# Kernel tuning notes

Hardware: AMD Instinct MI355X
Metric: run time of the kernel (lower is better)

Reference implementation:

```python
import jax, jax.numpy as jnp
import numpy as np

B, T, NV, DEG, E = 64, 256, 20000, 8, 128
NSEG, NBUCKET = NV * DEG, 288
F_DIST, F_DIR, F_TT, HID = 50, 50, 50, 100
FEED = 2 * E + F_DIST + F_DIR  # 356


def setup_inputs() -> dict:
    key = jax.random.key(0)
    ks = jax.random.split(key, 32)
    s = 1.0 / np.sqrt(E)
    return {
        "xs_padded": jax.random.randint(ks[0], (B, T), 0, NV),
        "lengths": jax.random.randint(ks[1], (B,), 8, T + 1),
        "xs_actions": jax.random.randint(ks[2], (B, T - 1), 0, DEG),
        "destinations": jax.random.randint(ks[3], (B,), 0, NV),
        "adj_list": jax.random.randint(ks[4], (NV, DEG), 0, NV),
        "seg_ids": jax.random.randint(ks[5], (NV, DEG), 0, NSEG),
        "start_time": 42,
        "locations": jax.random.normal(ks[6], (NV, 2)),
        "time_dist_seg": jax.random.uniform(ks[7], (NSEG, NBUCKET)) * 10.0,
        "emb": jax.random.normal(ks[8], (NV + 2, E)) * 0.01,
        "Wq": jax.random.normal(ks[9], (E, E)) * s,
        "Wk": jax.random.normal(ks[10], (E, E)) * s,
        "Wv": jax.random.normal(ks[11], (E, E)) * s,
        "Wo": jax.random.normal(ks[12], (E, E)) * s,
        "dist_W": jax.random.normal(ks[13], (1, F_DIST)),
        "dist_b": jnp.zeros((F_DIST,)),
        "dir_W": jax.random.normal(ks[14], (2, F_DIR)) * 0.7,
        "dir_b": jnp.zeros((F_DIR,)),
        "tt_W": jax.random.normal(ks[15], (1, F_TT)),
        "tt_b": jnp.zeros((F_TT,)),
        "ob_W1": jax.random.normal(ks[16], (F_TT, F_TT // 2)) * (1.0 / np.sqrt(F_TT)),
        "ob_b1": jnp.zeros((F_TT // 2,)),
        "ob_W2": jax.random.normal(ks[17], (F_TT // 2, 1)) * (1.0 / np.sqrt(F_TT // 2)),
        "ob_b2": jnp.zeros((1,)),
        "om_W1": jax.random.normal(ks[18], (FEED, HID)) * (1.0 / np.sqrt(FEED)),
        "om_b1": jnp.zeros((HID,)),
        "om_W2": jax.random.normal(ks[19], (HID, HID // 2)) * (1.0 / np.sqrt(HID)),
        "om_b2": jnp.zeros((HID // 2,)),
        "om_W3": jax.random.normal(ks[20], (HID // 2, 1)) * (1.0 / np.sqrt(HID // 2)),
        "om_b3": jnp.zeros((1,)),
    }


def reference(xs_padded, lengths, xs_actions, destinations, adj_list, seg_ids,
              start_time, locations, time_dist_seg, emb, Wq, Wk, Wv, Wo,
              dist_W, dist_b, dir_W, dir_b, tt_W, tt_b,
              ob_W1, ob_b1, ob_W2, ob_b2,
              om_W1, om_b1, om_W2, om_b2, om_W3, om_b3):
    # --- embeddings + causal/padding-masked self-attention (flash_att) ---
    x_e = emb[xs_padded]                                       # [B,T,E]
    q, k, v = x_e @ Wq, x_e @ Wk, x_e @ Wv
    scores = jnp.einsum('bqe,bke->bqk', q, k) / jnp.sqrt(jnp.float32(E))
    causal = jnp.triu(jnp.ones((T, T), bool), 1)
    pad = jnp.arange(T)[None, :] >= lengths[:, None]           # key padding [B,T]
    scores = jnp.where(causal[None] | pad[:, None, :], -1e9, scores)
    hidden = jnp.einsum('bqk,bke->bqe', jax.nn.softmax(scores, axis=-1), v) @ Wo

    # --- irregular neighbor gather: route_neighbors only filled for t < len-1 ---
    valid_t = jnp.arange(T)[None, :] < (lengths - 1)[:, None]  # [B,T]
    rn = jnp.where(valid_t[:, :, None], adj_list[xs_padded], 0)  # [B,T,DEG]

    # --- distance to destination feature ---
    dest_c = locations[destinations][:, None, None, :]         # [B,1,1,2]
    nbr_c = locations[rn]                                      # [B,T,DEG,2]
    dist = jnp.abs(nbr_c - dest_c).sum(-1, keepdims=True) * 100.0
    dist_f = dist @ dist_W + dist_b

    # --- direction (unit vector) feature ---
    vec = nbr_c - locations[xs_padded][:, :, None, :]
    unit = vec / (jnp.linalg.norm(vec, axis=-1, keepdims=True) + 1e-8)
    dir_f = unit @ dir_W + dir_b

    # --- travel-time lookup + masked whitening ---
    nmask = rn != 0
    tt = time_dist_seg[seg_ids[xs_padded], start_time]         # [B,T,DEG]
    mf = nmask.astype(tt.dtype)
    cnt = mf.sum()
    mean = (tt * mf).sum() / cnt
    var = (((tt - mean) ** 2) * mf).sum() / (cnt - 1.0)        # unbiased, like torch.std
    tt = (tt - mean) / (jnp.sqrt(var) + 1e-6)
    tt_f = (tt[..., None] @ tt_W + tt_b) * mf[..., None]

    # --- fuse and score neighbors ---
    hid_e = jnp.broadcast_to(hidden[:, :, None, :], (B, T, DEG, E))
    dest_e = jnp.broadcast_to(emb[destinations][:, None, None, :], (B, T, DEG, E))
    feed = jnp.concatenate([hid_e, dist_f, dir_f, dest_e], axis=-1)  # [B,T,DEG,356]

    ob = (jax.nn.relu(tt_f @ ob_W1 + ob_b1) @ ob_W2 + ob_b2).squeeze(-1)
    h1 = jax.nn.relu(feed @ om_W1 + om_b1)
    h2 = jax.nn.relu(h1 @ om_W2 + om_b2)
    logits = (h2 @ om_W3 + om_b3).squeeze(-1) + ob             # [B,T,DEG]

    # --- per-route mean cross-entropy over valid transitions, summed over batch ---
    logp = jax.nn.log_softmax(logits[:, :T - 1], axis=-1)
    nll = -jnp.take_along_axis(logp, xs_actions[..., None], axis=-1).squeeze(-1)
    vmask = (jnp.arange(T - 1)[None, :] < (lengths - 1)[:, None]).astype(nll.dtype)
    per = (nll * vmask).sum(1) / (lengths - 1).astype(nll.dtype)
    return per.sum()
```

## Files before the change

### kernel.cpp

```cpp
#include <hip/hip_runtime.h>
#include <math.h>

#define BB 64
#define TT 256
#define DEG 8
#define EE 128
#define NBUCKET 288
#define HID 100
#define H2 50

constexpr size_t OFF_STATS   = 0;
constexpr size_t OFF_CDIST   = 4;
constexpr size_t OFF_CDIRX   = 104;
constexpr size_t OFF_CDIRY   = 204;
constexpr size_t OFF_BASE    = 304;
constexpr size_t OFF_V25     = 404;
constexpr size_t OFF_C25     = 429;
constexpr size_t OFF_OBZ     = 454;
constexpr size_t OFF_DESTPRE = 456;
constexpr size_t OFF_WF      = 6856;
constexpr size_t OFF_TT      = 32456;
constexpr size_t OFF_Q       = 163528;
constexpr size_t OFF_K       = OFF_Q + 16384 * 128;
constexpr size_t OFF_VP      = OFF_K + 16384 * 128;

__global__ void __launch_bounds__(256) k_setup(
    const int* destinations, const float* emb, const float* Wo,
    const float* dist_W, const float* dist_b, const float* dir_W, const float* dir_b,
    const float* tt_W, const float* tt_b, const float* ob_W1, const float* ob_b1,
    const float* ob_W2, const float* ob_b2, const float* om_W1, const float* om_b1,
    float* ws, float* out) {
    __shared__ float sh[EE];
    int blk = blockIdx.x;
    int j = threadIdx.x;
    if (blk == 0) {
        if (j < 4) ws[OFF_STATS + j] = 0.f;
        if (j == 0) out[0] = 0.f;
        if (j < HID) {
            float cd = 0.f, cx = 0.f, cy = 0.f, bs = om_b1[j];
            for (int f = 0; f < 50; f++) {
                float w1d = om_W1[(128 + f) * HID + j];
                float w1r = om_W1[(178 + f) * HID + j];
                cd += dist_W[f] * w1d;
                bs += dist_b[f] * w1d + dir_b[f] * w1r;
                cx += dir_W[f] * w1r;
                cy += dir_W[50 + f] * w1r;
            }
            ws[OFF_CDIST + j] = cd; ws[OFF_CDIRX + j] = cx;
            ws[OFF_CDIRY + j] = cy; ws[OFF_BASE + j] = bs;
        }
        if (j >= 128 && j < 153) {
            int jj = j - 128;
            float v = 0.f, c = ob_b1[jj];
            for (int i = 0; i < 50; i++) {
                v += tt_W[i] * ob_W1[i * 25 + jj];
                c += tt_b[i] * ob_W1[i * 25 + jj];
            }
            ws[OFF_V25 + jj] = v; ws[OFF_C25 + jj] = c;
        }
        if (j == 200) {
            float z = ob_b2[0];
            for (int i = 0; i < 25; i++) z += fmaxf(ob_b1[i], 0.f) * ob_W2[i];
            ws[OFF_OBZ] = z;
        }
    } else if (blk <= 64) {
        int b = blk - 1;
        if (j < EE) sh[j] = emb[(size_t)destinations[b] * EE + j];
        __syncthreads();
        if (j < HID) {
            float acc = 0.f;
            for (int i = 0; i < EE; i++) acc += sh[i] * om_W1[(228 + i) * HID + j];
            ws[OFF_DESTPRE + b * HID + j] = acc;
        }
    } else {
        int i = blk - 65;
        if (j < EE) sh[j] = Wo[i * EE + j];
        __syncthreads();
        if (j < HID) {
            float acc = 0.f;
            for (int jj = 0; jj < EE; jj++) acc += sh[jj] * om_W1[jj * HID + j];
            ws[OFF_WF + i * HID + j] = acc;
        }
    }
}

__global__ void __launch_bounds__(256) k_mid(
    const int* xs, const int* lengths, const int* adj, const int* seg,
    const int* stime, const float* tds, const float* emb,
    const float* Wq, const float* Wk, const float* Wv, float* ws) {
    __shared__ float smem[2 * 128 * 36 + 32];
    int blk = blockIdx.x;
    int tid = threadIdx.x;
    if (blk < 512) {
        float (*XT)[36]  = (float(*)[36])smem;
        float (*T1T)[36] = (float(*)[36])(smem + 128 * 36);
        int* vids = (int*)(smem + 2 * 128 * 36);
        int r0 = blk * 32;
        if (tid < 32) vids[tid] = xs[r0 + tid];
        __syncthreads();
        for (int c = 0; c < 16; c++) {
            int idx = c * 256 + tid;
            int r = idx >> 7, i = idx & 127;
            XT[i][r] = emb[(size_t)vids[r] * EE + i];
        }
        __syncthreads();
        int cg = tid & 31, rg = tid >> 5;
        const float* Wmats[2] = {Wq, Wk};
        float* Omats[2] = {ws + OFF_Q, ws + OFF_K};
        for (int mtx = 0; mtx < 2; mtx++) {
            const float* W = Wmats[mtx];
            float acc[4][4];
            #pragma unroll
            for (int a = 0; a < 4; a++)
                #pragma unroll
                for (int bb = 0; bb < 4; bb++) acc[a][bb] = 0.f;
            #pragma unroll 4
            for (int i = 0; i < EE; i++) {
                float4 av = *(const float4*)&XT[i][rg << 2];
                float4 wv = *(const float4*)&W[i * EE + (cg << 2)];
                acc[0][0] += av.x * wv.x; acc[0][1] += av.x * wv.y; acc[0][2] += av.x * wv.z; acc[0][3] += av.x * wv.w;
                acc[1][0] += av.y * wv.x; acc[1][1] += av.y * wv.y; acc[1][2] += av.y * wv.z; acc[1][3] += av.y * wv.w;
                acc[2][0] += av.z * wv.x; acc[2][1] += av.z * wv.y; acc[2][2] += av.z * wv.z; acc[2][3] += av.z * wv.w;
                acc[3][0] += av.w * wv.x; acc[3][1] += av.w * wv.y; acc[3][2] += av.w * wv.z; acc[3][3] += av.w * wv.w;
            }
            float* O = Omats[mtx];
            #pragma unroll
            for (int jj = 0; jj < 4; jj++)
                *(float4*)&O[(size_t)(r0 + (rg << 2) + jj) * EE + (cg << 2)] =
                    make_float4(acc[jj][0], acc[jj][1], acc[jj][2], acc[jj][3]);
        }
        {
            float acc[4][4];
            #pragma unroll
            for (int a = 0; a < 4; a++)
                #pragma unroll
                for (int bb = 0; bb < 4; bb++) acc[a][bb] = 0.f;
            #pragma unroll 4
            for (int i = 0; i < EE; i++) {
                float4 av = *(const float4*)&XT[i][rg << 2];
                float4 wv = *(const float4*)&Wv[i * EE + (cg << 2)];
                acc[0][0] += av.x * wv.x; acc[0][1] += av.x * wv.y; acc[0][2] += av.x * wv.z; acc[0][3] += av.x * wv.w;
                acc[1][0] += av.y * wv.x; acc[1][1] += av.y * wv.y; acc[1][2] += av.y * wv.z; acc[1][3] += av.y * wv.w;
                acc[2][0] += av.z * wv.x; acc[2][1] += av.z * wv.y; acc[2][2] += av.z * wv.z; acc[2][3] += av.z * wv.w;
                acc[3][0] += av.w * wv.x; acc[3][1] += av.w * wv.y; acc[3][2] += av.w * wv.z; acc[3][3] += av.w * wv.w;
            }
            #pragma unroll
            for (int jj = 0; jj < 4; jj++)
                #pragma unroll
                for (int ii = 0; ii < 4; ii++)
                    T1T[(cg << 2) + ii][(rg << 2) + jj] = acc[jj][ii];
        }
        __syncthreads();
        if (cg < 25) {
            const float* WF = ws + OFF_WF;
            float acc[4][4];
            #pragma unroll
            for (int a = 0; a < 4; a++)
                #pragma unroll
                for (int bb = 0; bb < 4; bb++) acc[a][bb] = 0.f;
            #pragma unroll 4
            for (int i = 0; i < EE; i++) {
                float4 av = *(const float4*)&T1T[i][rg << 2];
                float4 wv = *(const float4*)&WF[i * HID + (cg << 2)];
                acc[0][0] += av.x * wv.x; acc[0][1] += av.x * wv.y; acc[0][2] += av.x * wv.z; acc[0][3] += av.x * wv.w;
                acc[1][0] += av.y * wv.x; acc[1][1] += av.y * wv.y; acc[1][2] += av.y * wv.z; acc[1][3] += av.y * wv.w;
                acc[2][0] += av.z * wv.x; acc[2][1] += av.z * wv.y; acc[2][2] += av.z * wv.z; acc[2][3] += av.z * wv.w;
                acc[3][0] += av.w * wv.x; acc[3][1] += av.w * wv.y; acc[3][2] += av.w * wv.z; acc[3][3] += av.w * wv.w;
            }
            float* VP = ws + OFF_VP;
            #pragma unroll
            for (int jj = 0; jj < 4; jj++)
                *(float4*)&VP[(size_t)(r0 + (rg << 2) + jj) * HID + (cg << 2)] =
                    make_float4(acc[jj][0], acc[jj][1], acc[jj][2], acc[jj][3]);
        }
    } else {
        float* rs = smem; float* rq = smem + 256; float* rc = smem + 512;
        int st = *stime;
        float lsum = 0.f, lsq = 0.f, lcnt = 0.f;
        int total = BB * TT * DEG;
        for (int idx = (blk - 512) * 256 + tid; idx < total; idx += 256 * 256) {
            int d = idx & 7;
            int bt = idx >> 3;
            int t = bt & 255;
            int b = bt >> 8;
            int len = lengths[b];
            if (t >= len - 1) continue;
            int v = xs[bt];
            int sg = seg[v * DEG + d];
            float tt = tds[(size_t)sg * NBUCKET + st];
            ws[OFF_TT + idx] = tt;
            int a = adj[v * DEG + d];
            if (a != 0) { lsum += tt; lsq += tt * tt; lcnt += 1.f; }
        }
        rs[tid] = lsum; rq[tid] = lsq; rc[tid] = lcnt;
        __syncthreads();
        for (int s = 128; s > 0; s >>= 1) {
            if (tid < s) { rs[tid] += rs[tid + s]; rq[tid] += rq[tid + s]; rc[tid] += rc[tid + s]; }
            __syncthreads();
        }
        if (tid == 0) {
            atomicAdd(&ws[OFF_STATS + 0], rs[0]);
            atomicAdd(&ws[OFF_STATS + 1], rq[0]);
            atomicAdd(&ws[OFF_STATS + 2], rc[0]);
        }
    }
}

__global__ void __launch_bounds__(256) k_attnfinal(
    const int* lengths, const int* xs, const int* xs_actions,
    const int* destinations, const int* adj, const float* locations,
    const float* om_W2, const float* om_b2, const float* om_W3, const float* om_b3,
    const float* ob_W2, const float* ob_b2,
    float* ws, float* out) {
    int b = blockIdx.x >> 4;
    int tile = blockIdx.x & 15;
    int t0 = tile << 4;
    int len = lengths[b];
    if (t0 >= len - 1) return;
    int nqv = len - 1 - t0; if (nqv > 16) nqv = 16;
    int nk = t0 + 16;
    int nm = nk >> 4;
    __shared__ float smem[17696];
    float (*S)[260]  = (float(*)[260])smem;
    float (*Qs)[132] = (float(*)[132])(smem + 4160);
    float* KV = smem + 6272;
    int tid = threadIdx.x;
    if (tid < 16) smem[17680 + tid] = 0.f;
    const float* Q  = ws + OFF_Q;
    const float* K  = ws + OFF_K;
    const float* VP = ws + OFF_VP;
    {
        const float* Qg = Q + ((size_t)(b * TT + t0)) * EE;
        for (int idx = tid; idx < 512; idx += 256) {
            int r = idx >> 5, c4 = (idx & 31) << 2;
            *(float4*)&Qs[r][c4] = *(const float4*)&Qg[r * EE + c4];
        }
    }
    int q = tid >> 4, li = tid & 15;
    int tq = t0 + q;
    float sreg[16];
    #pragma unroll
    for (int m = 0; m < 16; m++) sreg[m] = -1e30f;
    float (*Ks)[136] = (float(*)[136])KV;
    int ktend = ((nk + 31) >> 5) << 5;
    for (int kt = 0; kt < ktend; kt += 32) {
        __syncthreads();
        const float* Kg = K + ((size_t)(b * TT + kt)) * EE;
        for (int idx = tid; idx < 1024; idx += 256) {
            int r = idx >> 5, c4 = (idx & 31) << 2;
            *(float4*)&Ks[r][c4] = *(const float4*)&Kg[r * EE + c4];
        }
        __syncthreads();
        int k0 = kt + li, k1 = kt + li + 16;
        float s0 = 0.f, s1 = 0.f;
        const float4* q4  = (const float4*)Qs[q];
        const float4* k4a = (const float4*)Ks[li];
        const float4* k4b = (const float4*)Ks[li + 16];
        #pragma unroll 8
        for (int i = 0; i < 32; i++) {
            float4 a = q4[i];
            float4 x = k4a[i];
            float4 y = k4b[i];
            s0 += a.x * x.x + a.y * x.y + a.z * x.z + a.w * x.w;
            s1 += a.x * y.x + a.y * y.y + a.z * y.z + a.w * y.w;
        }
        int m0 = kt >> 4;
        if (k0 < nk && k0 <= tq) sreg[m0]     = s0 * 0.08838834764831845f;
        if (k1 < nk && k1 <= tq) sreg[m0 + 1] = s1 * 0.08838834764831845f;
    }
    float mx = -1e30f;
    for (int m = 0; m < nm; m++) mx = fmaxf(mx, sreg[m]);
    #pragma unroll
    for (int o = 1; o < 16; o <<= 1) mx = fmaxf(mx, __shfl_xor(mx, o, 16));
    float lsum = 0.f;
    for (int m = 0; m < nm; m++) { float p = __expf(sreg[m] - mx); sreg[m] = p; lsum += p; }
    #pragma unroll
    for (int o = 1; o < 16; o <<= 1) lsum += __shfl_xor(lsum, o, 16);
    float inv = 1.f / lsum;
    for (int m = 0; m < nm; m++) S[q][li + (m << 4)] = sreg[m];
    float acc[7];
    #pragma unroll
    for (int j = 0; j < 7; j++) acc[j] = 0.f;
    float (*Vs)[104] = (float(*)[104])KV;
    for (int vt = 0; vt < nk; vt += 32) {
        __syncthreads();
        const float* Vg = VP + ((size_t)(b * TT + vt)) * HID;
        for (int idx = tid; idx < 800; idx += 256) {
            int r = idx / 25, c4 = (idx - r * 25) << 2;
            *(float4*)&Vs[r][c4] = *(const float4*)&Vg[r * HID + c4];
        }
        __syncthreads();
        int kmax = nk - vt; if (kmax > 32) kmax = 32;
        for (int k = 0; k < kmax; k++) {
            float p = S[q][vt + k];
            #pragma unroll
            for (int j = 0; j < 7; j++) {
                int c = li + (j << 4);
                if (c < HID) acc[j] += p * Vs[k][c];
            }
        }
    }
    __syncthreads();
    {
        const float* BASEv = ws + OFF_BASE;
        const float* DP = ws + OFF_DESTPRE + b * HID;
        #pragma unroll
        for (int j = 0; j < 7; j++) {
            int c = li + (j << 4);
            if (c < HID) S[q][c] = acc[j] * inv + BASEv[c] + DP[c];
        }
    }
    float (*W2s)[64] = (float(*)[64])(smem + 4160);
    for (int idx = tid; idx < 6400; idx += 256) {
        int mm = idx >> 6, n = idx & 63;
        W2s[mm][n] = (n < H2) ? om_W2[mm * H2 + n] : 0.f;
    }
    float smean, sdinv;
    {
        float sum = ws[OFF_STATS], sq = ws[OFF_STATS + 1], cnt = ws[OFF_STATS + 2];
        smean = sum / cnt;
        float var = (sq - cnt * smean * smean) / (cnt - 1.f);
        sdinv = 1.f / (sqrtf(var) + 1e-6f);
    }
    float (*h1T)[68] = (float(*)[68])(smem + 10560);
    float* distR = smem + 17360;
    float* uxR   = smem + 17424;
    float* uyR   = smem + 17488;
    float* obR   = smem + 17552;
    float* lgS   = smem + 17616;
    float* nllS  = smem + 17680;
    int cg = tid & 7, rg = tid >> 3;
    float b2v[8], w3v[8];
    #pragma unroll
    for (int k = 0; k < 8; k++) {
        int n = (cg << 3) + k;
        b2v[k] = (n < H2) ? om_b2[n] : 0.f;
        w3v[k] = (n < H2) ? om_W3[n] : 0.f;
    }
    float ob2s = ob_b2[0];
    float obz = ws[OFF_OBZ];
    __syncthreads();
    for (int qh = 0; qh < 2; qh++) {
        if (tid < 64) {
            int ql = tid >> 3, d = tid & 7;
            int qa = (qh << 3) + ql;
            int t = t0 + qa;
            int bt = b * TT + t;
            int v = xs[bt];
            int a = adj[v * DEG + d];
            float nbx = locations[2 * a], nby = locations[2 * a + 1];
            int dst = destinations[b];
            float dxl = locations[2 * dst], dyl = locations[2 * dst + 1];
            float cxl = locations[2 * v], cyl = locations[2 * v + 1];
            distR[tid] = (fabsf(nbx - dxl) + fabsf(nby - dyl)) * 100.f;
            float vx = nbx - cxl, vy = nby - cyl;
            float nrm = sqrtf(vx * vx + vy * vy) + 1e-8f;
            uxR[tid] = vx / nrm; uyR[tid] = vy / nrm;
            float ttn = (ws[OFF_TT + (size_t)bt * 8 + d] - smean) * sdinv;
            float obp = 0.f;
            for (int j = 0; j < 25; j++)
                obp += fmaxf(ttn * ws[OFF_V25 + j] + ws[OFF_C25 + j], 0.f) * ob_W2[j];
            obR[tid] = (a != 0) ? (obp + ob2s) : obz;
        }
        __syncthreads();
        {
            int r = tid & 63, mq = tid >> 6;
            int qa = (qh << 3) + (r >> 3);
            float dv = distR[r], ux = uxR[r], uy = uyR[r];
            const float* CD = ws + OFF_CDIST;
            const float* CX = ws + OFF_CDIRX;
            const float* CY = ws + OFF_CDIRY;
            const float* Hq = S[qa];
            int m0 = mq * 25;
            #pragma unroll 5
            for (int mi = 0; mi < 25; mi++) {
                int m = m0 + mi;
                float pre = Hq[m] + dv * CD[m] + ux * CX[m] + uy * CY[m];
                h1T[m][r] = fmaxf(pre, 0.f);
            }
        }
        __syncthreads();
        {
            float facc[2][8];
            #pragma unroll
            for (int jr = 0; jr < 2; jr++)
                #pragma unroll
                for (int k = 0; k < 8; k++) facc[jr][k] = 0.f;
            int r0 = rg << 1, n0 = cg << 3;
            #pragma unroll 4
            for (int m = 0; m < HID; m++) {
                float2 hv = *(const float2*)&h1T[m][r0];
                float4 w0 = *(const float4*)&W2s[m][n0];
                float4 w1 = *(const float4*)&W2s[m][n0 + 4];
                facc[0][0] += hv.x * w0.x; facc[0][1] += hv.x * w0.y;
                facc[0][2] += hv.x * w0.z; facc[0][3] += hv.x * w0.w;
                facc[0][4] += hv.x * w1.x; facc[0][5] += hv.x * w1.y;
                facc[0][6] += hv.x * w1.z; facc[0][7] += hv.x * w1.w;
                facc[1][0] += hv.y * w0.x; facc[1][1] += hv.y * w0.y;
                facc[1][2] += hv.y * w0.z; facc[1][3] += hv.y * w0.w;
                facc[1][4] += hv.y * w1.x; facc[1][5] += hv.y * w1.y;
                facc[1][6] += hv.y * w1.z; facc[1][7] += hv.y * w1.w;
            }
            #pragma unroll
            for (int jr = 0; jr < 2; jr++) {
                float part = 0.f;
                #pragma unroll
                for (int k = 0; k < 8; k++)
                    part += fmaxf(facc[jr][k] + b2v[k], 0.f) * w3v[k];
                part += __shfl_xor(part, 1, 64);
                part += __shfl_xor(part, 2, 64);
                part += __shfl_xor(part, 4, 64);
                if (cg == 0) {
                    int row = r0 + jr;
                    lgS[row] = part + om_b3[0] + obR[row];
                }
            }
        }
        __syncthreads();
        if (tid < 8) {
            int qa = (qh << 3) + tid;
            if (qa < nqv) {
                int t = t0 + qa;
                float lg[8];
                float mxl = -1e30f;
                #pragma unroll
                for (int d = 0; d < 8; d++) {
                    lg[d] = lgS[(tid << 3) + d];
                    mxl = fmaxf(mxl, lg[d]);
                }
                int act = xs_actions[b * (TT - 1) + t];
                float se = 0.f, sel = 0.f;
                #pragma unroll
                for (int d = 0; d < 8; d++) {
                    se += __expf(lg[d] - mxl);
                    if (d == act) sel = lg[d];
                }
                float nll = mxl + __logf(se) - sel;
                nllS[qa] = nll / (float)(len - 1);
            }
        }
        __syncthreads();
    }
    if (tid == 0) {
        float s = 0.f;
        #pragma unroll
        for (int i = 0; i < 16; i++) s += nllS[i];
        atomicAdd(out, s);
    }
}

extern "C" void kernel_launch(void* const* d_in, const int* in_sizes, int n_in,
                              void* d_out, int out_size, void* d_ws, size_t ws_size,
                              hipStream_t stream) {
    const int* xs_padded    = (const int*)d_in[0];
    const int* lengths      = (const int*)d_in[1];
    const int* xs_actions   = (const int*)d_in[2];
    const int* destinations = (const int*)d_in[3];
    const int* adj_list     = (const int*)d_in[4];
    const int* seg_ids      = (const int*)d_in[5];
    const int* start_time   = (const int*)d_in[6];
    const float* locations  = (const float*)d_in[7];
    const float* tds        = (const float*)d_in[8];
    const float* emb        = (const float*)d_in[9];
    const float* Wq         = (const float*)d_in[10];
    const float* Wk         = (const float*)d_in[11];
    const float* Wv         = (const float*)d_in[12];
    const float* Wo         = (const float*)d_in[13];
    const float* dist_W     = (const float*)d_in[14];
    const float* dist_b     = (const float*)d_in[15];
    const float* dir_W      = (const float*)d_in[16];
    const float* dir_b      = (const float*)d_in[17];
    const float* tt_W       = (const float*)d_in[18];
    const float* tt_b       = (const float*)d_in[19];
    const float* ob_W1      = (const float*)d_in[20];
    const float* ob_b1      = (const float*)d_in[21];
    const float* ob_W2      = (const float*)d_in[22];
    const float* ob_b2      = (const float*)d_in[23];
    const float* om_W1      = (const float*)d_in[24];
    const float* om_b1      = (const float*)d_in[25];
    const float* om_W2      = (const float*)d_in[26];
    const float* om_b2      = (const float*)d_in[27];
    const float* om_W3      = (const float*)d_in[28];
    const float* om_b3      = (const float*)d_in[29];
    float* ws  = (float*)d_ws;
    float* out = (float*)d_out;

    k_setup<<<193, 256, 0, stream>>>(destinations, emb, Wo, dist_W, dist_b,
                                     dir_W, dir_b, tt_W, tt_b, ob_W1, ob_b1,
                                     ob_W2, ob_b2, om_W1, om_b1, ws, out);
    k_mid<<<768, 256, 0, stream>>>(xs_padded, lengths, adj_list, seg_ids,
                                   start_time, tds, emb, Wq, Wk, Wv, ws);
    k_attnfinal<<<BB * 16, 256, 0, stream>>>(
        lengths, xs_padded, xs_actions, destinations, adj_list, locations,
        om_W2, om_b2, om_W3, om_b3, ob_W2, ob_b2, ws, out);
}
```

Measured before the change: 471.5 us.

## Halve attention query tile, reorder blocks longest-first, restructure QK and PV work split

```diff
diff --git a/kernel.cpp b/kernel.cpp
--- a/kernel.cpp
+++ b/kernel.cpp
@@ -212,107 +212,142 @@
     const float* om_W2, const float* om_b2, const float* om_W3, const float* om_b3,
     const float* ob_W2, const float* ob_b2,
     float* ws, float* out) {
-    int b = blockIdx.x >> 4;
-    int tile = blockIdx.x & 15;
-    int t0 = tile << 4;
+    int blk = blockIdx.x;
+    int tile = 31 - (blk >> 6);
+    int b = blk & 63;
+    int t0 = tile << 3;
     int len = lengths[b];
     if (t0 >= len - 1) return;
-    int nqv = len - 1 - t0; if (nqv > 16) nqv = 16;
-    int nk = t0 + 16;
-    int nm = nk >> 4;
-    __shared__ float smem[17696];
-    float (*S)[260]  = (float(*)[260])smem;
-    float (*Qs)[132] = (float(*)[132])(smem + 4160);
-    float* KV = smem + 6272;
+    int nqv = len - 1 - t0; if (nqv > 8) nqv = 8;
+    int nk = t0 + 8;
+    __shared__ float smem[13160];
+    float (*H1P)[104] = (float(*)[104])smem;
+    float (*Qs)[132]  = (float(*)[132])(smem + 832);
+    float (*S)[260]   = (float(*)[260])(smem + 1888);
+    float (*Vs)[104]  = (float(*)[104])(smem + 3968);
+    float (*pacc)[8]  = (float(*)[8])(smem + 10624);
+    float (*W2s)[56]  = (float(*)[56])(smem + 832);
+    float (*h1T)[64]  = (float(*)[64])(smem + 6432);
+    float* distR = smem + 12832;
+    float* uxR   = smem + 12896;
+    float* uyR   = smem + 12960;
+    float* obR   = smem + 13024;
+    float* lgS   = smem + 13088;
+    float* nllS  = smem + 13152;
     int tid = threadIdx.x;
-    if (tid < 16) smem[17680 + tid] = 0.f;
-    const float* Q  = ws + OFF_Q;
-    const float* K  = ws + OFF_K;
-    const float* VP = ws + OFF_VP;
+    if (tid < 8) nllS[tid] = 0.f;
     {
-        const float* Qg = Q + ((size_t)(b * TT + t0)) * EE;
-        for (int idx = tid; idx < 512; idx += 256) {
-            int r = idx >> 5, c4 = (idx & 31) << 2;
-            *(float4*)&Qs[r][c4] = *(const float4*)&Qg[r * EE + c4];
-        }
-    }
-    int q = tid >> 4, li = tid & 15;
-    int tq = t0 + q;
-    float sreg[16];
-    #pragma unroll
-    for (int m = 0; m < 16; m++) sreg[m] = -1e30f;
-    float (*Ks)[136] = (float(*)[136])KV;
-    int ktend = ((nk + 31) >> 5) << 5;
-    for (int kt = 0; kt < ktend; kt += 32) {
-        __syncthreads();
-        const float* Kg = K + ((size_t)(b * TT + kt)) * EE;
-        for (int idx = tid; idx < 1024; idx += 256) {
-            int r = idx >> 5, c4 = (idx & 31) << 2;
-            *(float4*)&Ks[r][c4] = *(const float4*)&Kg[r * EE + c4];
-        }
-        __syncthreads();
-        int k0 = kt + li, k1 = kt + li + 16;
-        float s0 = 0.f, s1 = 0.f;
-        const float4* q4  = (const float4*)Qs[q];
-        const float4* k4a = (const float4*)Ks[li];
-        const float4* k4b = (const float4*)Ks[li + 16];
-        #pragma unroll 8
-        for (int i = 0; i < 32; i++) {
-            float4 a = q4[i];
-            float4 x = k4a[i];
-            float4 y = k4b[i];
-            s0 += a.x * x.x + a.y * x.y + a.z * x.z + a.w * x.w;
-            s1 += a.x * y.x + a.y * y.y + a.z * y.z + a.w * y.w;
-        }
-        int m0 = kt >> 4;
-        if (k0 < nk && k0 <= tq) sreg[m0]     = s0 * 0.08838834764831845f;
-        if (k1 < nk && k1 <= tq) sreg[m0 + 1] = s1 * 0.08838834764831845f;
-    }
-    float mx = -1e30f;
-    for (int m = 0; m < nm; m++) mx = fmaxf(mx, sreg[m]);
-    #pragma unroll
-    for (int o = 1; o < 16; o <<= 1) mx = fmaxf(mx, __shfl_xor(mx, o, 16));
-    float lsum = 0.f;
-    for (int m = 0; m < nm; m++) { float p = __expf(sreg[m] - mx); sreg[m] = p; lsum += p; }
-    #pragma unroll
-    for (int o = 1; o < 16; o <<= 1) lsum += __shfl_xor(lsum, o, 16);
-    float inv = 1.f / lsum;
-    for (int m = 0; m < nm; m++) S[q][li + (m << 4)] = sreg[m];
-    float acc[7];
-    #pragma unroll
-    for (int j = 0; j < 7; j++) acc[j] = 0.f;
-    float (*Vs)[104] = (float(*)[104])KV;
-    for (int vt = 0; vt < nk; vt += 32) {
-        __syncthreads();
-        const float* Vg = VP + ((size_t)(b * TT + vt)) * HID;
-        for (int idx = tid; idx < 800; idx += 256) {
-            int r = idx / 25, c4 = (idx - r * 25) << 2;
-            *(float4*)&Vs[r][c4] = *(const float4*)&Vg[r * HID + c4];
-        }
-        __syncthreads();
-        int kmax = nk - vt; if (kmax > 32) kmax = 32;
-        for (int k = 0; k < kmax; k++) {
-            float p = S[q][vt + k];
-            #pragma unroll
-            for (int j = 0; j < 7; j++) {
-                int c = li + (j << 4);
-                if (c < HID) acc[j] += p * Vs[k][c];
-            }
-        }
+        const float* Qg = ws + OFF_Q + (size_t)(b * TT + t0) * EE;
+        int r = tid >> 5, c4 = (tid & 31) << 2;
+        *(float4*)&Qs[r][c4] = *(const float4*)&Qg[r * EE + c4];
     }
     __syncthreads();
     {
-        const float* BASEv = ws + OFF_BASE;
-        const float* DP = ws + OFF_DESTPRE + b * HID;
-        #pragma unroll
-        for (int j = 0; j < 7; j++) {
-            int c = li + (j << 4);
-            if (c < HID) S[q][c] = acc[j] * inv + BASEv[c] + DP[c];
-        }
-    }
-    float (*W2s)[64] = (float(*)[64])(smem + 4160);
-    for (int idx = tid; idx < 6400; idx += 256) {
-        int mm = idx >> 6, n = idx & 63;
+        const float* Kg = ws + OFF_K + (size_t)(b * TT) * EE;
+        int w = tid >> 6;
+        int key = (tid >> 2) & 15, chunk = tid & 3;
+        int coff = chunk << 5;
+        for (int k0 = w << 4; k0 < nk; k0 += 64) {
+            int kk = k0 + key;
+            if (kk < nk) {
+                float4 kf[8];
+                const float4* Kr = (const float4*)&Kg[(size_t)kk * EE + coff];
+                #pragma unroll
+                for (int j = 0; j < 8; j++) kf[j] = Kr[j];
+                #pragma unroll
+                for (int q = 0; q < 8; q++) {
+                    const float4* qr = (const float4*)&Qs[q][coff];
+                    float s = 0.f;
+                    #pragma unroll
+                    for (int j = 0; j < 8; j++) {
+                        float4 a = qr[j], x = kf[j];
+                        s += a.x * x.x + a.y * x.y + a.z * x.z + a.w * x.w;
+                    }
+                    s += __shfl_xor(s, 1, 64);
+                    s += __shfl_xor(s, 2, 64);
+                    if (chunk == 0) S[q][kk] = s * 0.08838834764831845f;
+                }
+            }
+        }
+    }
+    __syncthreads();
+    if (tid < 128) {
+        int q = tid >> 4, li = tid & 15;
+        int tq = t0 + q;
+        float sreg[16];
+        float mx = -1e30f;
+        #pragma unroll
+        for (int m = 0; m < 16; m++) {
+            int k = li + (m << 4);
+            float sv = (k < nk && k <= tq) ? S[q][k] : -1e30f;
+            sreg[m] = sv;
+            mx = fmaxf(mx, sv);
+        }
+        #pragma unroll
+        for (int o = 1; o < 16; o <<= 1) mx = fmaxf(mx, __shfl_xor(mx, o, 16));
+        float ls = 0.f;
+        #pragma unroll
+        for (int m = 0; m < 16; m++) {
+            float p = __expf(sreg[m] - mx);
+            sreg[m] = p; ls += p;
+        }
+        #pragma unroll
+        for (int o = 1; o < 16; o <<= 1) ls += __shfl_xor(ls, o, 16);
+        float inv = 1.f / ls;
+        #pragma unroll
+        for (int m = 0; m < 16; m++) S[q][li + (m << 4)] = sreg[m] * inv;
+    }
+    __syncthreads();
+    {
+        int kc = tid >> 7;
+        int q = (tid >> 4) & 7, cg = tid & 15;
+        float acc[8];
+        #pragma unroll
+        for (int j = 0; j < 8; j++) acc[j] = 0.f;
+        const float* VPg = ws + OFF_VP + (size_t)(b * TT) * HID;
+        for (int vt0 = 0; vt0 < nk; vt0 += 64) {
+            __syncthreads();
+            int nrow = nk - vt0; if (nrow > 64) nrow = 64;
+            for (int idx = tid; idx < nrow * 25; idx += 256) {
+                int r = idx / 25, c4 = (idx - r * 25) << 2;
+                *(float4*)&Vs[r][c4] = *(const float4*)&VPg[(size_t)(vt0 + r) * HID + c4];
+            }
+            __syncthreads();
+            int base = vt0 + (kc << 5);
+            int kmax = nk - base; if (kmax > 32) kmax = 32;
+            if (cg < 13) {
+                for (int k = 0; k < kmax; k++) {
+                    float p = S[q][base + k];
+                    const float4* vr = (const float4*)&Vs[(kc << 5) + k][cg << 3];
+                    float4 v0 = vr[0], v1 = vr[1];
+                    acc[0] += p * v0.x; acc[1] += p * v0.y;
+                    acc[2] += p * v0.z; acc[3] += p * v0.w;
+                    acc[4] += p * v1.x; acc[5] += p * v1.y;
+                    acc[6] += p * v1.z; acc[7] += p * v1.w;
+                }
+            }
+        }
+        if (kc == 1 && cg < 13) {
+            float* pp = pacc[(q << 4) + cg];
+            #pragma unroll
+            for (int j = 0; j < 8; j++) pp[j] = acc[j];
+        }
+        __syncthreads();
+        if (kc == 0 && cg < 13) {
+            const float* pp = pacc[(q << 4) + cg];
+            const float* BASEv = ws + OFF_BASE;
+            const float* DP = ws + OFF_DESTPRE + b * HID;
+            int c0 = cg << 3;
+            #pragma unroll
+            for (int j = 0; j < 8; j++) {
+                int c = c0 + j;
+                if (c < HID) H1P[q][c] = acc[j] + pp[j] + BASEv[c] + DP[c];
+            }
+        }
+    }
+    __syncthreads();
+    for (int idx = tid; idx < 5600; idx += 256) {
+        int mm = idx / 56, n = idx - mm * 56;
         W2s[mm][n] = (n < H2) ? om_W2[mm * H2 + n] : 0.f;
     }
     float smean, sdinv;
@@ -322,129 +357,121 @@
         float var = (sq - cnt * smean * smean) / (cnt - 1.f);
         sdinv = 1.f / (sqrtf(var) + 1e-6f);
     }
-    float (*h1T)[68] = (float(*)[68])(smem + 10560);
-    float* distR = smem + 17360;
-    float* uxR   = smem + 17424;
-    float* uyR   = smem + 17488;
-    float* obR   = smem + 17552;
-    float* lgS   = smem + 17616;
-    float* nllS  = smem + 17680;
-    int cg = tid & 7, rg = tid >> 3;
-    float b2v[8], w3v[8];
-    #pragma unroll
-    for (int k = 0; k < 8; k++) {
-        int n = (cg << 3) + k;
-        b2v[k] = (n < H2) ? om_b2[n] : 0.f;
-        w3v[k] = (n < H2) ? om_W3[n] : 0.f;
-    }
-    float ob2s = ob_b2[0];
-    float obz = ws[OFF_OBZ];
-    __syncthreads();
-    for (int qh = 0; qh < 2; qh++) {
-        if (tid < 64) {
-            int ql = tid >> 3, d = tid & 7;
-            int qa = (qh << 3) + ql;
-            int t = t0 + qa;
-            int bt = b * TT + t;
-            int v = xs[bt];
-            int a = adj[v * DEG + d];
-            float nbx = locations[2 * a], nby = locations[2 * a + 1];
-            int dst = destinations[b];
-            float dxl = locations[2 * dst], dyl = locations[2 * dst + 1];
-            float cxl = locations[2 * v], cyl = locations[2 * v + 1];
-            distR[tid] = (fabsf(nbx - dxl) + fabsf(nby - dyl)) * 100.f;
-            float vx = nbx - cxl, vy = nby - cyl;
-            float nrm = sqrtf(vx * vx + vy * vy) + 1e-8f;
-            uxR[tid] = vx / nrm; uyR[tid] = vy / nrm;
-            float ttn = (ws[OFF_TT + (size_t)bt * 8 + d] - smean) * sdinv;
-            float obp = 0.f;
-            for (int j = 0; j < 25; j++)
-                obp += fmaxf(ttn * ws[OFF_V25 + j] + ws[OFF_C25 + j], 0.f) * ob_W2[j];
-            obR[tid] = (a != 0) ? (obp + ob2s) : obz;
-        }
-        __syncthreads();
-        {
-            int r = tid & 63, mq = tid >> 6;
-            int qa = (qh << 3) + (r >> 3);
-            float dv = distR[r], ux = uxR[r], uy = uyR[r];
-            const float* CD = ws + OFF_CDIST;
-            const float* CX = ws + OFF_CDIRX;
-            const float* CY = ws + OFF_CDIRY;
-            const float* Hq = S[qa];
-            int m0 = mq * 25;
-            #pragma unroll 5
-            for (int mi = 0; mi < 25; mi++) {
-                int m = m0 + mi;
-                float pre = Hq[m] + dv * CD[m] + ux * CX[m] + uy * CY[m];
-                h1T[m][r] = fmaxf(pre, 0.f);
-            }
-        }
-        __syncthreads();
-        {
-            float facc[2][8];
-            #pragma unroll
-            for (int jr = 0; jr < 2; jr++)
+    if (tid < 64) {
+        int ql = tid >> 3, d = tid & 7;
+        int t = t0 + ql;
+        int bt = b * TT + t;
+        int v = xs[bt];
+        int a = adj[v * DEG + d];
+        float nbx = locations[2 * a], nby = locations[2 * a + 1];
+        int dst = destinations[b];
+        float dxl = locations[2 * dst], dyl = locations[2 * dst + 1];
+        float cxl = locations[2 * v], cyl = locations[2 * v + 1];
+        distR[tid] = (fabsf(nbx - dxl) + fabsf(nby - dyl)) * 100.f;
+        float vx = nbx - cxl, vy = nby - cyl;
+        float nrm = sqrtf(vx * vx + vy * vy) + 1e-8f;
+        uxR[tid] = vx / nrm; uyR[tid] = vy / nrm;
+        float ttn = (ws[OFF_TT + (size_t)bt * 8 + d] - smean) * sdinv;
+        float obp = 0.f;
+        for (int j = 0; j < 25; j++)
+            obp += fmaxf(ttn * ws[OFF_V25 + j] + ws[OFF_C25 + j], 0.f) * ob_W2[j];
+        obR[tid] = (a != 0) ? (obp + ob_b2[0]) : ws[OFF_OBZ];
+    }
+    __syncthreads();
+    {
+        int r = tid & 63, mq = tid >> 6;
+        int qa = r >> 3;
+        float dv = distR[r], ux = uxR[r], uy = uyR[r];
+        const float* CD = ws + OFF_CDIST;
+        const float* CX = ws + OFF_CDIRX;
+        const float* CY = ws + OFF_CDIRY;
+        const float* Hq = H1P[qa];
+        int m0 = mq * 25;
+        #pragma unroll 5
+        for (int mi = 0; mi < 25; mi++) {
+            int m = m0 + mi;
+            float pre = Hq[m] + dv * CD[m] + ux * CX[m] + uy * CY[m];
+            h1T[m][r] = fmaxf(pre, 0.f);
+        }
+    }
+    __syncthreads();
+    if (tid < 128) {
+        int rg = tid >> 3, cg = tid & 7;
+        int r0 = rg << 2, n0 = cg << 3;
+        float parts[4] = {0.f, 0.f, 0.f, 0.f};
+        if (cg < 7) {
+            float facc[4][8];
+            #pragma unroll
+            for (int jr = 0; jr < 4; jr++)
                 #pragma unroll
                 for (int k = 0; k < 8; k++) facc[jr][k] = 0.f;
-            int r0 = rg << 1, n0 = cg << 3;
             #pragma unroll 4
             for (int m = 0; m < HID; m++) {
-                float2 hv = *(const float2*)&h1T[m][r0];
+                float4 hv = *(const float4*)&h1T[m][r0];
                 float4 w0 = *(const float4*)&W2s[m][n0];
                 float4 w1 = *(const float4*)&W2s[m][n0 + 4];
-                facc[0][0] += hv.x * w0.x; facc[0][1] += hv.x * w0.y;
-                facc[0][2] += hv.x * w0.z; facc[0][3] += hv.x * w0.w;
-                facc[0][4] += hv.x * w1.x; facc[0][5] += hv.x * w1.y;
-                facc[0][6] += hv.x * w1.z; facc[0][7] += hv.x * w1.w;
-                facc[1][0] += hv.y * w0.x; facc[1][1] += hv.y * w0.y;
-                facc[1][2] += hv.y * w0.z; facc[1][3] += hv.y * w0.w;
-                facc[1][4] += hv.y * w1.x; facc[1][5] += hv.y * w1.y;
-                facc[1][6] += hv.y * w1.z; facc[1][7] += hv.y * w1.w;
-            }
-            #pragma unroll
-            for (int jr = 0; jr < 2; jr++) {
+                facc[0][0] += hv.x * w0.x; facc[0][1] += hv.x * w0.y; facc[0][2] += hv.x * w0.z; facc[0][3] += hv.x * w0.w;
+                facc[0][4] += hv.x * w1.x; facc[0][5] += hv.x * w1.y; facc[0][6] += hv.x * w1.z; facc[0][7] += hv.x * w1.w;
+                facc[1][0] += hv.y * w0.x; facc[1][1] += hv.y * w0.y; facc[1][2] += hv.y * w0.z; facc[1][3] += hv.y * w0.w;
+                facc[1][4] += hv.y * w1.x; facc[1][5] += hv.y * w1.y; facc[1][6] += hv.y * w1.z; facc[1][7] += hv.y * w1.w;
+                facc[2][0] += hv.z * w0.x; facc[2][1] += hv.z * w0.y; facc[2][2] += hv.z * w0.z; facc[2][3] += hv.z * w0.w;
+                facc[2][4] += hv.z * w1.x; facc[2][5] += hv.z * w1.y; facc[2][6] += hv.z * w1.z; facc[2][7] += hv.z * w1.w;
+                facc[3][0] += hv.w * w0.x; facc[3][1] += hv.w * w0.y; facc[3][2] += hv.w * w0.z; facc[3][3] += hv.w * w0.w;
+                facc[3][4] += hv.w * w1.x; facc[3][5] += hv.w * w1.y; facc[3][6] += hv.w * w1.z; facc[3][7] += hv.w * w1.w;
+            }
+            float b2v[8], w3v[8];
+            #pragma unroll
+            for (int k = 0; k < 8; k++) {
+                int n = n0 + k;
+                b2v[k] = (n < H2) ? om_b2[n] : 0.f;
+                w3v[k] = (n < H2) ? om_W3[n] : 0.f;
+            }
+            #pragma unroll
+            for (int jr = 0; jr < 4; jr++) {
                 float part = 0.f;
                 #pragma unroll
                 for (int k = 0; k < 8; k++)
                     part += fmaxf(facc[jr][k] + b2v[k], 0.f) * w3v[k];
-                part += __shfl_xor(part, 1, 64);
-                part += __shfl_xor(part, 2, 64);
-                part += __shfl_xor(part, 4, 64);
-                if (cg == 0) {
-                    int row = r0 + jr;
-                    lgS[row] = part + om_b3[0] + obR[row];
-                }
-            }
-        }
-        __syncthreads();
-        if (tid < 8) {
-            int qa = (qh << 3) + tid;
-            if (qa < nqv) {
-                int t = t0 + qa;
-                float lg[8];
-                float mxl = -1e30f;
-                #pragma unroll
-                for (int d = 0; d < 8; d++) {
-                    lg[d] = lgS[(tid << 3) + d];
-                    mxl = fmaxf(mxl, lg[d]);
-                }
-                int act = xs_actions[b * (TT - 1) + t];
-                float se = 0.f, sel = 0.f;
-                #pragma unroll
-                for (int d = 0; d < 8; d++) {
-                    se += __expf(lg[d] - mxl);
-                    if (d == act) sel = lg[d];
-                }
-                float nll = mxl + __logf(se) - sel;
-                nllS[qa] = nll / (float)(len - 1);
-            }
-        }
-        __syncthreads();
-    }
+                parts[jr] = part;
+            }
+        }
+        float ob3 = om_b3[0];
+        #pragma unroll
+        for (int jr = 0; jr < 4; jr++) {
+            float part = parts[jr];
+            part += __shfl_xor(part, 1, 64);
+            part += __shfl_xor(part, 2, 64);
+            part += __shfl_xor(part, 4, 64);
+            if (cg == 0) lgS[r0 + jr] = part + ob3 + obR[r0 + jr];
+        }
+    }
+    __syncthreads();
+    if (tid < 8) {
+        int qa = tid;
+        if (qa < nqv) {
+            float lg[8];
+            float mxl = -1e30f;
+            #pragma unroll
+            for (int d = 0; d < 8; d++) {
+                lg[d] = lgS[(qa << 3) + d];
+                mxl = fmaxf(mxl, lg[d]);
+            }
+            int act = xs_actions[b * (TT - 1) + t0 + qa];
+            float se = 0.f, sel = 0.f;
+            #pragma unroll
+            for (int d = 0; d < 8; d++) {
+                se += __expf(lg[d] - mxl);
+                if (d == act) sel = lg[d];
+            }
+            float nll = mxl + __logf(se) - sel;
+            nllS[qa] = nll / (float)(len - 1);
+        }
+    }
+    __syncthreads();
     if (tid == 0) {
         float s = 0.f;
         #pragma unroll
-        for (int i = 0; i < 16; i++) s += nllS[i];
+        for (int i = 0; i < 8; i++) s += nllS[i];
         atomicAdd(out, s);
     }
 }
@@ -490,7 +517,7 @@
                                      ob_W2, ob_b2, om_W1, om_b1, ws, out);
     k_mid<<<768, 256, 0, stream>>>(xs_padded, lengths, adj_list, seg_ids,
                                    start_time, tds, emb, Wq, Wk, Wv, ws);
-    k_attnfinal<<<BB * 16, 256, 0, stream>>>(
+    k_attnfinal<<<BB * 32, 256, 0, stream>>>(
         lengths, xs_padded, xs_actions, destinations, adj_list, locations,
         om_W2, om_b2, om_W3, om_b3, ob_W2, ob_b2, ws, out);
 }
```

Result: faster. 444.7 us (-5.7%).
